# Kernel optimization log

Measured on AMD Instinct MI355X. Metric: run time of the kernel, lower is better.

## Reference

```python
import jax, jax.numpy as jnp
import numpy as np


NUM_HEADS = 16


def setup_inputs() -> dict:
    key = jax.random.key(0)
    ks = jax.random.split(key, 6)
    B, Sq, Skv, DQ, DKV = 2, 1024, 4096, 1024, 768
    return {
        "x_q": jax.random.normal(ks[0], (B, Sq, DQ), jnp.float32),
        "x_kv": jax.random.normal(ks[1], (B, Skv, DKV), jnp.float32),
        "Wq": jax.random.normal(ks[2], (DQ, DQ), jnp.float32) * 0.02,
        "Wk": jax.random.normal(ks[3], (DQ, DKV), jnp.float32) * 0.02,
        "Wv": jax.random.normal(ks[4], (DQ, DKV), jnp.float32) * 0.02,
        "Wo": jax.random.normal(ks[5], (DQ, DQ), jnp.float32) * 0.02,
    }


def _split_heads(x):
    # Faithful to torch view(B, H, S, hd): a pure reshape, NOT a transpose.
    B, S, D = x.shape
    return x.reshape(B, NUM_HEADS, S, D // NUM_HEADS)


def reference(x_q, x_kv, Wq, Wk, Wv, Wo):
    head_dim = x_q.shape[-1] // NUM_HEADS
    # torch Linear: y = x @ W.T, weight shape (out, in)
    Q = _split_heads(jnp.einsum("bsd,od->bso", x_q, Wq))   # (B,H,Sq',hd)
    K = _split_heads(jnp.einsum("bsd,od->bso", x_kv, Wk))  # (B,H,Skv',hd)
    V = _split_heads(jnp.einsum("bsd,od->bso", x_kv, Wv))
    # Scale is 1/head_dim (not 1/sqrt), faithful to the source.
    scores = jnp.einsum("bhqd,bhkd->bhqk", Q, K) / head_dim
    attn = jax.nn.softmax(scores, axis=-1)
    out = jnp.einsum("bhqk,bhkd->bhqd", attn, V)  # (B,H,Sq',hd)
    B, Sq, DQ = x_q.shape
    out = out.transpose(0, 2, 1, 3).reshape(B, Sq, DQ)
    return jnp.einsum("bsd,od->bso", out, Wo)
```

## Files before the change

### kernel.cpp

```cpp
#include <hip/hip_runtime.h>
#include <hip/hip_bf16.h>
#include <cstdint>

#define THREADS 256

typedef __attribute__((ext_vector_type(8))) short bf16x8;
typedef __attribute__((ext_vector_type(4))) float f32x4;
typedef __attribute__((ext_vector_type(2))) unsigned int u32x2;

__device__ __forceinline__ void load_lds16(const void* g, void* l) {
    __builtin_amdgcn_global_load_lds(
        (const __attribute__((address_space(1))) unsigned int*)g,
        (__attribute__((address_space(3))) unsigned int*)l, 16, 0, 0);
}

__device__ __forceinline__ unsigned short f2bf(float x) {
    __hip_bfloat16 hb = __float2bfloat16(x);
    return *(unsigned short*)&hb;
}

__device__ __forceinline__ unsigned cvt_pk_bf16(float lo, float hi) {
    unsigned r;
    asm("v_cvt_pk_bf16_f32 %0, %1, %2" : "=v"(r) : "v"(lo), "v"(hi));
    return r;
}

__device__ __forceinline__ float fexp2(float x) {
#if __has_builtin(__builtin_amdgcn_exp2f)
    return __builtin_amdgcn_exp2f(x);
#else
    return exp2f(x);
#endif
}

__device__ __forceinline__ void swap32(unsigned& lo, unsigned& hi) {
#if __has_builtin(__builtin_amdgcn_permlane32_swap)
    u32x2 r = __builtin_amdgcn_permlane32_swap(lo, hi, false, false);
    lo = r[0]; hi = r[1];
#else
    unsigned plo = (unsigned)__shfl_xor((int)lo, 32, 64);
    unsigned phi = (unsigned)__shfl_xor((int)hi, 32, 64);
    bool up = (threadIdx.x & 32) != 0;
    unsigned nlo = up ? phi : lo;
    unsigned nhi = up ? hi : plo;
    lo = nlo; hi = nhi;
#endif
}

__global__ __launch_bounds__(THREADS)
void cast_inputs(const float* __restrict__ xq, const float* __restrict__ xkv,
                 const float* __restrict__ wq, const float* __restrict__ wk,
                 const float* __restrict__ wv, const float* __restrict__ wo,
                 unsigned short* __restrict__ oq, unsigned short* __restrict__ okv,
                 unsigned short* __restrict__ owq, unsigned short* __restrict__ owk,
                 unsigned short* __restrict__ owv, unsigned short* __restrict__ owo) {
    const unsigned n0 = 524288, n1 = 1572864, n2 = 262144, n3 = 196608, n4 = 196608;
    unsigned i = blockIdx.x * THREADS + threadIdx.x;
    const float* src; unsigned short* dst; unsigned off;
    if (i < n0)                    { src = xq;  dst = oq;  off = i; }
    else if (i < n0+n1)            { src = xkv; dst = okv; off = i - n0; }
    else if (i < n0+n1+n2)         { src = wq;  dst = owq; off = i - n0 - n1; }
    else if (i < n0+n1+n2+n3)      { src = wk;  dst = owk; off = i - n0 - n1 - n2; }
    else if (i < n0+n1+n2+n3+n4)   { src = wv;  dst = owv; off = i - n0 - n1 - n2 - n3; }
    else                           { src = wo;  dst = owo; off = i - n0 - n1 - n2 - n3 - n4; }
    float4 v = *(const float4*)(src + (size_t)off * 4);
    ushort4 o;
    o.x = f2bf(v.x); o.y = f2bf(v.y); o.z = f2bf(v.z); o.w = f2bf(v.w);
    *(ushort4*)(dst + (size_t)off * 4) = o;
}

__global__ __launch_bounds__(THREADS)
void gemm_proj(const unsigned short* __restrict__ xkv, const unsigned short* __restrict__ wkv,
               unsigned short* __restrict__ Kn, unsigned short* __restrict__ Vt,
               const unsigned short* __restrict__ xq, const unsigned short* __restrict__ wq,
               unsigned short* __restrict__ Qout) {
    __shared__ __align__(16) unsigned short As[128 * 64];
    __shared__ __align__(16) unsigned short Bs[128 * 64];

    const int t    = threadIdx.x;
    const int w    = t >> 6;
    const int lane = t & 63;
    const int l15  = lane & 15;
    const int quad = lane >> 4;
    const int wm   = w & 1;
    const int wn   = w >> 1;

    if (blockIdx.x < 1024) {
        const int bN = (blockIdx.x & 15) * 128;
        const int bM = (blockIdx.x >> 4) * 128;
        const int Kd = 768;

        const int srow = t >> 3;
        const int scol = ((t & 7) ^ ((t >> 4) & 7)) << 3;
        const unsigned short* ga = xkv + (size_t)(bM + srow) * Kd + scol;
        const unsigned short* gb = wkv + (size_t)(bN + srow) * Kd + scol;
        const int lbase = w * 512;

        const int xr = (l15 >> 1) & 7;
        int aoff[2][4], boff[2][4];
#pragma unroll
        for (int kk = 0; kk < 2; ++kk)
#pragma unroll
            for (int mt = 0; mt < 4; ++mt) {
                aoff[kk][mt] = (wm * 64 + mt * 16 + l15) * 64 + (((kk * 4 + quad) ^ xr) << 3);
                boff[kk][mt] = (wn * 64 + mt * 16 + l15) * 64 + (((kk * 4 + quad) ^ xr) << 3);
            }

        f32x4 acc[4][4];
#pragma unroll
        for (int mt = 0; mt < 4; ++mt)
#pragma unroll
            for (int nt = 0; nt < 4; ++nt)
#pragma unroll
                for (int r = 0; r < 4; ++r) acc[mt][nt][r] = 0.f;

        for (int k0 = 0; k0 < Kd; k0 += 64) {
            __syncthreads();
#pragma unroll
            for (int it = 0; it < 4; ++it) {
                load_lds16(ga + (size_t)it * 32 * Kd + k0, &As[lbase + it * 2048]);
                load_lds16(gb + (size_t)it * 32 * Kd + k0, &Bs[lbase + it * 2048]);
            }
            __syncthreads();

#pragma unroll
            for (int kk = 0; kk < 2; ++kk) {
                bf16x8 af[4], bf[4];
#pragma unroll
                for (int mt = 0; mt < 4; ++mt) af[mt] = *(const bf16x8*)&As[aoff[kk][mt]];
#pragma unroll
                for (int nt = 0; nt < 4; ++nt) bf[nt] = *(const bf16x8*)&Bs[boff[kk][nt]];
#pragma unroll
                for (int mt = 0; mt < 4; ++mt)
#pragma unroll
                    for (int nt = 0; nt < 4; ++nt)
                        acc[mt][nt] = __builtin_amdgcn_mfma_f32_16x16x32_bf16(af[mt], bf[nt], acc[mt][nt], 0, 0, 0);
            }
        }

        const int rbase = bM + wm * 64;
        const int b  = rbase >> 12;
        const int h  = (rbase & 4095) >> 8;
        if (bN < 1024) {
            const int G = (bN + wn * 64) >> 6;
            unsigned short* kp = Kn + (size_t)(b * 16 + h) * 262144 + (size_t)G * 256 * 64 + l15;
#pragma unroll
            for (int mt = 0; mt < 4; ++mt)
#pragma unroll
                for (int r = 0; r < 4; ++r) {
                    int u = (rbase & 255) + mt * 16 + quad * 4 + r;
                    unsigned short* cp = kp + (size_t)u * 64;
#pragma unroll
                    for (int nt = 0; nt < 4; ++nt) cp[nt * 16] = f2bf(acc[mt][nt][r]);
                }
        } else {
            const int Gv = (bN - 1024 + wn * 64) >> 6;
            unsigned short* vp = Vt + (size_t)(b * 16 + h) * 262144 + (size_t)Gv * 256;
#pragma unroll
            for (int nt = 0; nt < 4; ++nt) {
                int d = nt * 16 + l15;
#pragma unroll
                for (int mt = 0; mt < 4; ++mt) {
                    int u = (rbase & 255) + mt * 16 + quad * 4;
                    ushort4 pk;
                    pk.x = f2bf(acc[mt][nt][0]);
                    pk.y = f2bf(acc[mt][nt][1]);
                    pk.z = f2bf(acc[mt][nt][2]);
                    pk.w = f2bf(acc[mt][nt][3]);
                    *(ushort4*)(vp + (size_t)d * 4096 + u) = pk;
                }
            }
        }
    } else {
        const int id = blockIdx.x - 1024;
        const int bN = (id & 15) * 64;
        const int bM = (id >> 4) * 64;
        const int Kd = 1024, N = 1024;

        const int srow = t >> 3;
        const int scol = ((t & 7) ^ ((t >> 3) & 7)) << 3;
        const unsigned short* ga = xq + (size_t)(bM + srow) * Kd + scol;
        const unsigned short* gb = wq + (size_t)(bN + srow) * Kd + scol;
        const int lbase = w * 512;

        int aoff[2][2], boff[2][2];
#pragma unroll
        for (int kk = 0; kk < 2; ++kk)
#pragma unroll
            for (int mt = 0; mt < 2; ++mt) {
                aoff[kk][mt] = (wm * 32 + mt * 16 + l15) * 64 + (((kk * 4 + quad) ^ (l15 & 7)) << 3);
                boff[kk][mt] = (wn * 32 + mt * 16 + l15) * 64 + (((kk * 4 + quad) ^ (l15 & 7)) << 3);
            }

        f32x4 acc[2][2];
#pragma unroll
        for (int mt = 0; mt < 2; ++mt)
#pragma unroll
            for (int nt = 0; nt < 2; ++nt)
#pragma unroll
                for (int r = 0; r < 4; ++r) acc[mt][nt][r] = 0.f;

        for (int k0 = 0; k0 < Kd; k0 += 64) {
            __syncthreads();
#pragma unroll
            for (int it = 0; it < 2; ++it) {
                load_lds16(ga + (size_t)it * 32 * Kd + k0, &As[lbase + it * 2048]);
                load_lds16(gb + (size_t)it * 32 * Kd + k0, &Bs[lbase + it * 2048]);
            }
            __syncthreads();

#pragma unroll
            for (int kk = 0; kk < 2; ++kk) {
                bf16x8 af[2], bf[2];
#pragma unroll
                for (int mt = 0; mt < 2; ++mt) af[mt] = *(const bf16x8*)&As[aoff[kk][mt]];
#pragma unroll
                for (int nt = 0; nt < 2; ++nt) bf[nt] = *(const bf16x8*)&Bs[boff[kk][nt]];
#pragma unroll
                for (int mt = 0; mt < 2; ++mt)
#pragma unroll
                    for (int nt = 0; nt < 2; ++nt)
                        acc[mt][nt] = __builtin_amdgcn_mfma_f32_16x16x32_bf16(af[mt], bf[nt], acc[mt][nt], 0, 0, 0);
            }
        }

#pragma unroll
        for (int mt = 0; mt < 2; ++mt)
#pragma unroll
            for (int r = 0; r < 4; ++r) {
                int row = bM + wm * 32 + mt * 16 + quad * 4 + r;
                int col = bN + wn * 32 + l15;
                unsigned short* cp = Qout + (size_t)row * N + col;
#pragma unroll
                for (int nt = 0; nt < 2; ++nt) cp[nt * 16] = f2bf(acc[mt][nt][r]);
            }
    }
}

template <bool OUTF32>
__global__ __launch_bounds__(THREADS)
void gemm_bf16_nt64(const unsigned short* __restrict__ A, const unsigned short* __restrict__ W,
                    void* __restrict__ Cout, int M, int N, int Kd) {
    __shared__ __align__(16) unsigned short As[64 * 64];
    __shared__ __align__(16) unsigned short Bs[64 * 64];

    const int t    = threadIdx.x;
    const int w    = t >> 6;
    const int lane = t & 63;
    const int l15  = lane & 15;
    const int quad = lane >> 4;
    const int wm   = w & 1;
    const int wn   = w >> 1;
    const int bM = blockIdx.y * 64;
    const int bN = blockIdx.x * 64;

    const int srow = t >> 3;
    const int scol = ((t & 7) ^ ((t >> 3) & 7)) << 3;
    const unsigned short* ga = A + (size_t)(bM + srow) * Kd + scol;
    const unsigned short* gb = W + (size_t)(bN + srow) * Kd + scol;
    const int lbase = w * 512;

    int aoff[2][2], boff[2][2];
#pragma unroll
    for (int kk = 0; kk < 2; ++kk)
#pragma unroll
        for (int mt = 0; mt < 2; ++mt) {
            aoff[kk][mt] = (wm * 32 + mt * 16 + l15) * 64 + (((kk * 4 + quad) ^ (l15 & 7)) << 3);
            boff[kk][mt] = (wn * 32 + mt * 16 + l15) * 64 + (((kk * 4 + quad) ^ (l15 & 7)) << 3);
        }

    f32x4 acc[2][2];
#pragma unroll
    for (int mt = 0; mt < 2; ++mt)
#pragma unroll
        for (int nt = 0; nt < 2; ++nt)
#pragma unroll
            for (int r = 0; r < 4; ++r) acc[mt][nt][r] = 0.f;

    for (int k0 = 0; k0 < Kd; k0 += 64) {
        __syncthreads();
#pragma unroll
        for (int it = 0; it < 2; ++it) {
            load_lds16(ga + (size_t)it * 32 * Kd + k0, &As[lbase + it * 2048]);
            load_lds16(gb + (size_t)it * 32 * Kd + k0, &Bs[lbase + it * 2048]);
        }
        __syncthreads();

#pragma unroll
        for (int kk = 0; kk < 2; ++kk) {
            bf16x8 af[2], bf[2];
#pragma unroll
            for (int mt = 0; mt < 2; ++mt) af[mt] = *(const bf16x8*)&As[aoff[kk][mt]];
#pragma unroll
            for (int nt = 0; nt < 2; ++nt) bf[nt] = *(const bf16x8*)&Bs[boff[kk][nt]];
#pragma unroll
            for (int mt = 0; mt < 2; ++mt)
#pragma unroll
                for (int nt = 0; nt < 2; ++nt)
                    acc[mt][nt] = __builtin_amdgcn_mfma_f32_16x16x32_bf16(af[mt], bf[nt], acc[mt][nt], 0, 0, 0);
        }
    }

#pragma unroll
    for (int mt = 0; mt < 2; ++mt)
#pragma unroll
        for (int r = 0; r < 4; ++r) {
            int row = bM + wm * 32 + mt * 16 + quad * 4 + r;
            int col = bN + wn * 32 + l15;
            if (OUTF32) {
                float* cp = (float*)Cout + (size_t)row * N + col;
#pragma unroll
                for (int nt = 0; nt < 2; ++nt) cp[nt * 16] = acc[mt][nt][r];
            } else {
                unsigned short* cp = (unsigned short*)Cout + (size_t)row * N + col;
#pragma unroll
                for (int nt = 0; nt < 2; ++nt) cp[nt * 16] = f2bf(acc[mt][nt][r]);
            }
        }
}

__global__ __launch_bounds__(THREADS, 2)
void attn_mfma10(const unsigned short* __restrict__ Q, const unsigned short* __restrict__ K,
                 const unsigned short* __restrict__ Vt, unsigned short* __restrict__ AO) {
    extern __shared__ __align__(16) unsigned short sm[];
    unsigned short* Ks = sm;
    unsigned short* Vs = sm + 8192;
    float* OS = (float*)sm;
    float* Lw = (float*)(sm + 26624);

    const int bid  = blockIdx.x;
    const int slot = bid >> 3;
    const int qq   = slot & 15;
    const int hh   = (bid & 7) + 8 * (slot >> 4);
    const int q0 = qq * 64;
    const int h  = hh & 15;
    const int b  = hh >> 4;

    const int t    = threadIdx.x;
    const int w    = t >> 6;
    const int lane = t & 63;
    const int l15  = lane & 15;
    const int quad = lane >> 4;
    const int qsel = quad & 1;

    const unsigned short* Qh = Q + (size_t)b * 1048576 + (size_t)h * 65536 + (size_t)q0 * 64;
    const unsigned short* Kh = K + (size_t)b * 4194304 + (size_t)h * 262144;
    const unsigned short* Vh = Vt + (size_t)(b * 16 + h) * 262144;

    bf16x8 Qb[4][2];
#pragma unroll
    for (int qt = 0; qt < 4; ++qt)
#pragma unroll
        for (int kk = 0; kk < 2; ++kk)
            Qb[qt][kk] = *(const bf16x8*)(Qh + (size_t)(qt * 16 + l15) * 64 + kk * 32 + quad * 8);

    const unsigned short* gKw = Kh + (size_t)(w * 32 + (lane >> 3)) * 64
                                   + (((lane & 7) ^ ((lane >> 3) & 7)) << 3);
    const unsigned short* gVw = Vh + (size_t)(lane >> 2) * 4096 + w * 32
                                   + (((lane & 3) ^ ((lane >> 2) & 3)) << 3);
    const int ldsK = w * 2048;
    const int ldsV = w * 2048;

    int koff[2][2];
#pragma unroll
    for (int kvt = 0; kvt < 2; ++kvt)
#pragma unroll
        for (int kk = 0; kk < 2; ++kk)
            koff[kvt][kk] = (w * 32 + kvt * 16 + l15) * 64 + (((kk * 4 + quad) ^ (l15 & 7)) << 3);
    int voff[4];
#pragma unroll
    for (int dt = 0; dt < 4; ++dt)
        voff[dt] = w * 2048 + (dt * 16 + l15) * 32 + ((quad ^ (l15 & 3)) << 3);

    f32x4 Oacc[4][4];
#pragma unroll
    for (int qt = 0; qt < 4; ++qt)
#pragma unroll
        for (int dt = 0; dt < 4; ++dt)
#pragma unroll
            for (int r = 0; r < 4; ++r) Oacc[qt][dt][r] = 0.f;
    float lsum[4] = {0.f, 0.f, 0.f, 0.f};

    const float e2s = 0.022542110013890053f;

#pragma unroll
    for (int it = 0; it < 4; ++it)
        load_lds16(gKw + it * 512, &Ks[ldsK + it * 512]);
#pragma unroll
    for (int it = 0; it < 4; ++it)
        load_lds16(gVw + (size_t)it * 65536, &Vs[ldsV + it * 512]);

    for (int kc = 0; kc < 32; ++kc) {
        const int kn = (kc + 1) & 31;

        asm volatile("s_waitcnt vmcnt(4)" ::: "memory");

        bf16x8 ka0 = *(const bf16x8*)&Ks[koff[0][0]];
        bf16x8 kb0 = *(const bf16x8*)&Ks[koff[0][1]];
        bf16x8 ka1 = *(const bf16x8*)&Ks[koff[1][0]];
        bf16x8 kb1 = *(const bf16x8*)&Ks[koff[1][1]];
        asm volatile("s_waitcnt lgkmcnt(0)" ::: "memory");
#pragma unroll
        for (int it = 0; it < 4; ++it)
            load_lds16(gKw + (size_t)kn * 8192 + it * 512, &Ks[ldsK + it * 512]);

        bf16x8 Pa[4];
#pragma unroll
        for (int qt = 0; qt < 4; ++qt) {
            f32x4 S0 = {0.f, 0.f, 0.f, 0.f};
            S0 = __builtin_amdgcn_mfma_f32_16x16x32_bf16(ka0, Qb[qt][0], S0, 0, 0, 0);
            S0 = __builtin_amdgcn_mfma_f32_16x16x32_bf16(kb0, Qb[qt][1], S0, 0, 0, 0);
            f32x4 S1 = {0.f, 0.f, 0.f, 0.f};
            S1 = __builtin_amdgcn_mfma_f32_16x16x32_bf16(ka1, Qb[qt][0], S1, 0, 0, 0);
            S1 = __builtin_amdgcn_mfma_f32_16x16x32_bf16(kb1, Qb[qt][1], S1, 0, 0, 0);
            float p0 = fexp2(S0[0] * e2s);
            float p1 = fexp2(S0[1] * e2s);
            float p2 = fexp2(S0[2] * e2s);
            float p3 = fexp2(S0[3] * e2s);
            float p4 = fexp2(S1[0] * e2s);
            float p5 = fexp2(S1[1] * e2s);
            float p6 = fexp2(S1[2] * e2s);
            float p7 = fexp2(S1[3] * e2s);
            lsum[qt] += ((p0 + p1) + (p2 + p3)) + ((p4 + p5) + (p6 + p7));
            unsigned ca = cvt_pk_bf16(p0, p1);
            unsigned cb = cvt_pk_bf16(p2, p3);
            unsigned cc = cvt_pk_bf16(p4, p5);
            unsigned cd = cvt_pk_bf16(p6, p7);
            swap32(ca, cc);
            swap32(cb, cd);
            unsigned r0 = (unsigned)__shfl_xor((int)(qsel ? ca : cc), 16, 64);
            unsigned r1 = (unsigned)__shfl_xor((int)(qsel ? cb : cd), 16, 64);
            union { unsigned u[4]; bf16x8 v; } pk_;
            pk_.u[0] = qsel ? r0 : ca;
            pk_.u[1] = qsel ? r1 : cb;
            pk_.u[2] = qsel ? cc : r0;
            pk_.u[3] = qsel ? cd : r1;
            Pa[qt] = pk_.v;
        }

        asm volatile("s_waitcnt vmcnt(4)" ::: "memory");

        bf16x8 Vf[4];
#pragma unroll
        for (int dt = 0; dt < 4; ++dt) Vf[dt] = *(const bf16x8*)&Vs[voff[dt]];
        asm volatile("s_waitcnt lgkmcnt(0)" ::: "memory");
#pragma unroll
        for (int it = 0; it < 4; ++it)
            load_lds16(gVw + (size_t)kn * 128 + (size_t)it * 65536, &Vs[ldsV + it * 512]);

        __builtin_amdgcn_s_setprio(1);
#pragma unroll
        for (int qt = 0; qt < 4; ++qt)
#pragma unroll
            for (int dt = 0; dt < 4; ++dt)
                Oacc[qt][dt] = __builtin_amdgcn_mfma_f32_16x16x32_bf16(Pa[qt], Vf[dt], Oacc[qt][dt], 0, 0, 0);
        __builtin_amdgcn_s_setprio(0);
    }

#pragma unroll
    for (int qt = 0; qt < 4; ++qt) {
        float v = lsum[qt];
        v += __shfl_xor(v, 16);
        v += __shfl_xor(v, 32);
        lsum[qt] = v;
    }
    __syncthreads();
    if (lane < 16) {
#pragma unroll
        for (int qt = 0; qt < 4; ++qt)
            Lw[w * 64 + qt * 16 + lane] = lsum[qt];
    }
    if (w > 0) {
        float* myOS = OS + (w - 1) * 4352;
#pragma unroll
        for (int qt = 0; qt < 4; ++qt)
#pragma unroll
            for (int dt = 0; dt < 4; ++dt)
                *(f32x4*)&myOS[(dt * 16 + l15) * 68 + qt * 16 + quad * 4] = Oacc[qt][dt];
    }
    __syncthreads();
    if (w == 0) {
#pragma unroll
        for (int qt = 0; qt < 4; ++qt) {
            f32x4 lv = *(const f32x4*)&Lw[qt * 16 + quad * 4];
            lv += *(const f32x4*)&Lw[64 + qt * 16 + quad * 4];
            lv += *(const f32x4*)&Lw[128 + qt * 16 + quad * 4];
            lv += *(const f32x4*)&Lw[192 + qt * 16 + quad * 4];
            f32x4 inv;
#pragma unroll
            for (int r = 0; r < 4; ++r) inv[r] = 1.0f / lv[r];
#pragma unroll
            for (int dt = 0; dt < 4; ++dt) {
                f32x4 o = Oacc[qt][dt];
                int os = (dt * 16 + l15) * 68 + qt * 16 + quad * 4;
                o += *(const f32x4*)&OS[os];
                o += *(const f32x4*)&OS[4352 + os];
                o += *(const f32x4*)&OS[8704 + os];
#pragma unroll
                for (int r = 0; r < 4; ++r) {
                    int q = qt * 16 + quad * 4 + r;
                    AO[(size_t)b * 1048576 + (size_t)(q0 + q) * 1024 + (h << 6) + dt * 16 + l15]
                        = f2bf(o[r] * inv[r]);
                }
            }
        }
    }
}

extern "C" void kernel_launch(void* const* d_in, const int* in_sizes, int n_in,
                              void* d_out, int out_size, void* d_ws, size_t ws_size,
                              hipStream_t stream) {
    const float* x_q  = (const float*)d_in[0];
    const float* x_kv = (const float*)d_in[1];
    const float* Wq   = (const float*)d_in[2];
    const float* Wk   = (const float*)d_in[3];
    const float* Wv   = (const float*)d_in[4];
    const float* Wo   = (const float*)d_in[5];
    float* out = (float*)d_out;

    unsigned short* base   = (unsigned short*)d_ws;
    unsigned short* xq_bf  = base;
    unsigned short* xkv_bf = base + 2097152;
    unsigned short* wq_bf  = base + 8388608;
    unsigned short* wk_bf  = base + 9437184;
    unsigned short* wv_bf  = base + 10223616;
    unsigned short* wo_bf  = base + 11010048;
    unsigned short* Qw     = base + 12058624;
    unsigned short* Kw     = base + 14155776;
    unsigned short* AOb    = base + 22544384;
    unsigned short* Vtw    = base + 30932992;

    dim3 blk(THREADS);
    cast_inputs<<<dim3(11776), blk, 0, stream>>>(x_q, x_kv, Wq, Wk, Wv, Wo,
                                                 xq_bf, xkv_bf, wq_bf, wk_bf, wv_bf, wo_bf);
    gemm_proj<<<dim3(1536), blk, 0, stream>>>(xkv_bf, wk_bf, Kw, Vtw, xq_bf, wq_bf, Qw);
    attn_mfma10<<<dim3(512), blk, 54272, stream>>>(Qw, Kw, Vtw, AOb);
    gemm_bf16_nt64<true><<<dim3(16, 32), blk, 0, stream>>>(AOb, wo_bf, (void*)out, 2048, 1024, 1024);
}
```

Measured before the change: 204.8 us.

## Split attention KV range in two with separate combine kernel

Attention now splits the KV sequence into two halves, launching 1024 blocks instead of 512. Each block writes unnormalized fp32 partial outputs and row sums to workspace, and a new combine kernel sums the halves, normalizes, and writes bf16. The change also reduces LDS use through a tree reduction across warps, raises launch bounds to 4 blocks per SM, and replaces the shuffle-based P repacking with permlane16 swaps. The aim is better occupancy and wave fill on the GPU, paid for with an extra launch and fp32 partial traffic that reuses the input-cast workspace region.

After: 278.3 us. +35.9%, slower.

```diff
diff --git a/kernel.cpp b/kernel.cpp
--- a/kernel.cpp
+++ b/kernel.cpp
@@ -44,6 +44,20 @@
     unsigned nlo = up ? phi : lo;
     unsigned nhi = up ? hi : plo;
     lo = nlo; hi = nhi;
+#endif
+}
+
+__device__ __forceinline__ void swap16(unsigned& a, unsigned& c) {
+#if __has_builtin(__builtin_amdgcn_permlane16_swap)
+    u32x2 r = __builtin_amdgcn_permlane16_swap(a, c, false, false);
+    a = r[0]; c = r[1];
+#else
+    unsigned as = (unsigned)__shfl_xor((int)a, 16, 64);
+    unsigned cs = (unsigned)__shfl_xor((int)c, 16, 64);
+    bool odd = (threadIdx.x & 16) != 0;
+    unsigned na = odd ? cs : a;
+    unsigned nc = odd ? c  : as;
+    a = na; c = nc;
 #endif
 }
 
@@ -319,33 +333,37 @@
         }
 }
 
-__global__ __launch_bounds__(THREADS, 2)
-void attn_mfma10(const unsigned short* __restrict__ Q, const unsigned short* __restrict__ K,
-                 const unsigned short* __restrict__ Vt, unsigned short* __restrict__ AO) {
+__global__ __launch_bounds__(THREADS, 4)
+void attn_mfma12(const unsigned short* __restrict__ Q, const unsigned short* __restrict__ K,
+                 const unsigned short* __restrict__ Vt,
+                 float* __restrict__ Opart, float* __restrict__ lpart) {
     extern __shared__ __align__(16) unsigned short sm[];
     unsigned short* Ks = sm;
     unsigned short* Vs = sm + 8192;
     float* OS = (float*)sm;
-    float* Lw = (float*)(sm + 26624);
+    float* Lw = OS + 8704;
 
     const int bid  = blockIdx.x;
-    const int slot = bid >> 3;
+    const int kvh  = bid >> 9;
+    const int bid9 = bid & 511;
+    const int slot = bid9 >> 3;
     const int qq   = slot & 15;
-    const int hh   = (bid & 7) + 8 * (slot >> 4);
+    const int hh   = (bid9 & 7) + 8 * (slot >> 4);
     const int q0 = qq * 64;
     const int h  = hh & 15;
     const int b  = hh >> 4;
+    const int pslot = kvh * 512 + bid9;
 
     const int t    = threadIdx.x;
     const int w    = t >> 6;
     const int lane = t & 63;
     const int l15  = lane & 15;
     const int quad = lane >> 4;
-    const int qsel = quad & 1;
 
     const unsigned short* Qh = Q + (size_t)b * 1048576 + (size_t)h * 65536 + (size_t)q0 * 64;
-    const unsigned short* Kh = K + (size_t)b * 4194304 + (size_t)h * 262144;
-    const unsigned short* Vh = Vt + (size_t)(b * 16 + h) * 262144;
+    const unsigned short* Kh = K + (size_t)b * 4194304 + (size_t)h * 262144
+                                 + (size_t)kvh * 131072;
+    const unsigned short* Vh = Vt + (size_t)(b * 16 + h) * 262144 + kvh * 2048;
 
     bf16x8 Qb[4][2];
 #pragma unroll
@@ -390,8 +408,8 @@
     for (int it = 0; it < 4; ++it)
         load_lds16(gVw + (size_t)it * 65536, &Vs[ldsV + it * 512]);
 
-    for (int kc = 0; kc < 32; ++kc) {
-        const int kn = (kc + 1) & 31;
+    for (int kc = 0; kc < 16; ++kc) {
+        const int kn = (kc + 1) & 15;
 
         asm volatile("s_waitcnt vmcnt(4)" ::: "memory");
 
@@ -428,13 +446,13 @@
             unsigned cd = cvt_pk_bf16(p6, p7);
             swap32(ca, cc);
             swap32(cb, cd);
-            unsigned r0 = (unsigned)__shfl_xor((int)(qsel ? ca : cc), 16, 64);
-            unsigned r1 = (unsigned)__shfl_xor((int)(qsel ? cb : cd), 16, 64);
+            swap16(ca, cc);
+            swap16(cb, cd);
             union { unsigned u[4]; bf16x8 v; } pk_;
-            pk_.u[0] = qsel ? r0 : ca;
-            pk_.u[1] = qsel ? r1 : cb;
-            pk_.u[2] = qsel ? cc : r0;
-            pk_.u[3] = qsel ? cd : r1;
+            pk_.u[0] = ca;
+            pk_.u[1] = cb;
+            pk_.u[2] = cc;
+            pk_.u[3] = cd;
             Pa[qt] = pk_.v;
         }
 
@@ -470,8 +488,8 @@
         for (int qt = 0; qt < 4; ++qt)
             Lw[w * 64 + qt * 16 + lane] = lsum[qt];
     }
-    if (w > 0) {
-        float* myOS = OS + (w - 1) * 4352;
+    if (w == 1 || w == 3) {
+        float* myOS = OS + (w >> 1) * 4352;
 #pragma unroll
         for (int qt = 0; qt < 4; ++qt)
 #pragma unroll
@@ -479,32 +497,70 @@
                 *(f32x4*)&myOS[(dt * 16 + l15) * 68 + qt * 16 + quad * 4] = Oacc[qt][dt];
     }
     __syncthreads();
+    if (w == 0 || w == 2) {
+        const float* srcOS = OS + (w >> 1) * 4352;
+#pragma unroll
+        for (int qt = 0; qt < 4; ++qt)
+#pragma unroll
+            for (int dt = 0; dt < 4; ++dt)
+                Oacc[qt][dt] += *(const f32x4*)&srcOS[(dt * 16 + l15) * 68 + qt * 16 + quad * 4];
+    }
+    __syncthreads();
+    if (w == 2) {
+#pragma unroll
+        for (int qt = 0; qt < 4; ++qt)
+#pragma unroll
+            for (int dt = 0; dt < 4; ++dt)
+                *(f32x4*)&OS[(dt * 16 + l15) * 68 + qt * 16 + quad * 4] = Oacc[qt][dt];
+    }
+    __syncthreads();
     if (w == 0) {
+        float* pO = Opart + (size_t)pslot * 4096;
+        float* pl = lpart + (size_t)pslot * 64;
 #pragma unroll
         for (int qt = 0; qt < 4; ++qt) {
             f32x4 lv = *(const f32x4*)&Lw[qt * 16 + quad * 4];
             lv += *(const f32x4*)&Lw[64 + qt * 16 + quad * 4];
             lv += *(const f32x4*)&Lw[128 + qt * 16 + quad * 4];
             lv += *(const f32x4*)&Lw[192 + qt * 16 + quad * 4];
-            f32x4 inv;
-#pragma unroll
-            for (int r = 0; r < 4; ++r) inv[r] = 1.0f / lv[r];
+            if (l15 == 0) *(f32x4*)&pl[qt * 16 + quad * 4] = lv;
 #pragma unroll
             for (int dt = 0; dt < 4; ++dt) {
                 f32x4 o = Oacc[qt][dt];
-                int os = (dt * 16 + l15) * 68 + qt * 16 + quad * 4;
-                o += *(const f32x4*)&OS[os];
-                o += *(const f32x4*)&OS[4352 + os];
-                o += *(const f32x4*)&OS[8704 + os];
-#pragma unroll
-                for (int r = 0; r < 4; ++r) {
-                    int q = qt * 16 + quad * 4 + r;
-                    AO[(size_t)b * 1048576 + (size_t)(q0 + q) * 1024 + (h << 6) + dt * 16 + l15]
-                        = f2bf(o[r] * inv[r]);
-                }
-            }
-        }
-    }
+                o += *(const f32x4*)&OS[(dt * 16 + l15) * 68 + qt * 16 + quad * 4];
+#pragma unroll
+                for (int r = 0; r < 4; ++r)
+                    pO[(size_t)(qt * 16 + quad * 4 + r) * 64 + dt * 16 + l15] = o[r];
+            }
+        }
+    }
+}
+
+__global__ __launch_bounds__(THREADS)
+void attn_combine(const float* __restrict__ Op, const float* __restrict__ lp,
+                  unsigned short* __restrict__ AO) {
+    const int t    = threadIdx.x;
+    const int s9   = blockIdx.x >> 2;
+    const int part = blockIdx.x & 3;
+    const int q    = part * 16 + (t >> 4);
+    const int dg   = (t & 15) << 2;
+    const int slot = s9 >> 3;
+    const int qq   = slot & 15;
+    const int hh   = (s9 & 7) + 8 * (slot >> 4);
+    const int q0 = qq * 64;
+    const int h  = hh & 15;
+    const int b  = hh >> 4;
+
+    size_t off = (size_t)s9 * 4096 + q * 64 + dg;
+    f32x4 a = *(const f32x4*)&Op[off];
+    f32x4 c = *(const f32x4*)&Op[2097152 + off];
+    float inv = 1.0f / (lp[s9 * 64 + q] + lp[32768 + s9 * 64 + q]);
+    ushort4 o;
+    o.x = f2bf((a[0] + c[0]) * inv);
+    o.y = f2bf((a[1] + c[1]) * inv);
+    o.z = f2bf((a[2] + c[2]) * inv);
+    o.w = f2bf((a[3] + c[3]) * inv);
+    *(ushort4*)(AO + (size_t)b * 1048576 + (size_t)(q0 + q) * 1024 + (h << 6) + dg) = o;
 }
 
 extern "C" void kernel_launch(void* const* d_in, const int* in_sizes, int n_in,
@@ -530,10 +586,14 @@
     unsigned short* AOb    = base + 22544384;
     unsigned short* Vtw    = base + 30932992;
 
+    float* Opart = (float*)d_ws;
+    float* lpart = (float*)(base + 24641536);
+
     dim3 blk(THREADS);
     cast_inputs<<<dim3(11776), blk, 0, stream>>>(x_q, x_kv, Wq, Wk, Wv, Wo,
                                                  xq_bf, xkv_bf, wq_bf, wk_bf, wv_bf, wo_bf);
     gemm_proj<<<dim3(1536), blk, 0, stream>>>(xkv_bf, wk_bf, Kw, Vtw, xq_bf, wq_bf, Qw);
-    attn_mfma10<<<dim3(512), blk, 54272, stream>>>(Qw, Kw, Vtw, AOb);
+    attn_mfma12<<<dim3(1024), blk, 35840, stream>>>(Qw, Kw, Vtw, Opart, lpart);
+    attn_combine<<<dim3(2048), blk, 0, stream>>>(Opart, lpart, AOb);
     gemm_bf16_nt64<true><<<dim3(16, 32), blk, 0, stream>>>(AOb, wo_bf, (void*)out, 2048, 1024, 1024);
 }
```

## Double-buffer K/V LDS tiles in attention and use permlane16 swap for P

Applied to the files above, without the earlier changes.

The attention kernel moves from single-buffered K and V LDS tiles to two buffers, prefetching chunk kc+2 while chunk kc is computed, and relaxes the vmcnt waits to match. It also replaces the shfl_xor-plus-select repacking of the probability fragments with a permlane16_swap. The aim is to hide global-to-LDS latency and cut cross-lane shuffle cost. LDS per block grows from 54 KB to 64 KB, which may limit occupancy to two blocks per CU, and the epilogue reuses the same shared memory.

Measured after the change: 194.8 us. 1.05x faster.

```diff
diff --git a/kernel.cpp b/kernel.cpp
--- a/kernel.cpp
+++ b/kernel.cpp
@@ -44,6 +44,20 @@
     unsigned nlo = up ? phi : lo;
     unsigned nhi = up ? hi : plo;
     lo = nlo; hi = nhi;
+#endif
+}
+
+__device__ __forceinline__ void swap16(unsigned& a, unsigned& c) {
+#if __has_builtin(__builtin_amdgcn_permlane16_swap)
+    u32x2 r = __builtin_amdgcn_permlane16_swap(a, c, false, false);
+    a = r[0]; c = r[1];
+#else
+    unsigned as = (unsigned)__shfl_xor((int)a, 16, 64);
+    unsigned cs = (unsigned)__shfl_xor((int)c, 16, 64);
+    bool odd = (threadIdx.x & 16) != 0;
+    unsigned na = odd ? cs : a;
+    unsigned nc = odd ? c  : as;
+    a = na; c = nc;
 #endif
 }
 
@@ -320,11 +334,9 @@
 }
 
 __global__ __launch_bounds__(THREADS, 2)
-void attn_mfma10(const unsigned short* __restrict__ Q, const unsigned short* __restrict__ K,
+void attn_mfma13(const unsigned short* __restrict__ Q, const unsigned short* __restrict__ K,
                  const unsigned short* __restrict__ Vt, unsigned short* __restrict__ AO) {
     extern __shared__ __align__(16) unsigned short sm[];
-    unsigned short* Ks = sm;
-    unsigned short* Vs = sm + 8192;
     float* OS = (float*)sm;
     float* Lw = (float*)(sm + 26624);
 
@@ -341,7 +353,6 @@
     const int lane = t & 63;
     const int l15  = lane & 15;
     const int quad = lane >> 4;
-    const int qsel = quad & 1;
 
     const unsigned short* Qh = Q + (size_t)b * 1048576 + (size_t)h * 65536 + (size_t)q0 * 64;
     const unsigned short* Kh = K + (size_t)b * 4194304 + (size_t)h * 262144;
@@ -385,24 +396,33 @@
 
 #pragma unroll
     for (int it = 0; it < 4; ++it)
-        load_lds16(gKw + it * 512, &Ks[ldsK + it * 512]);
+        load_lds16(gKw + it * 512, &sm[ldsK + it * 512]);
 #pragma unroll
     for (int it = 0; it < 4; ++it)
-        load_lds16(gVw + (size_t)it * 65536, &Vs[ldsV + it * 512]);
+        load_lds16(gVw + (size_t)it * 65536, &sm[16384 + ldsV + it * 512]);
+#pragma unroll
+    for (int it = 0; it < 4; ++it)
+        load_lds16(gKw + 8192 + it * 512, &sm[8192 + ldsK + it * 512]);
+#pragma unroll
+    for (int it = 0; it < 4; ++it)
+        load_lds16(gVw + 128 + (size_t)it * 65536, &sm[24576 + ldsV + it * 512]);
 
     for (int kc = 0; kc < 32; ++kc) {
-        const int kn = (kc + 1) & 31;
-
-        asm volatile("s_waitcnt vmcnt(4)" ::: "memory");
-
-        bf16x8 ka0 = *(const bf16x8*)&Ks[koff[0][0]];
-        bf16x8 kb0 = *(const bf16x8*)&Ks[koff[0][1]];
-        bf16x8 ka1 = *(const bf16x8*)&Ks[koff[1][0]];
-        bf16x8 kb1 = *(const bf16x8*)&Ks[koff[1][1]];
+        const int buf = kc & 1;
+        const int kn2 = (kc + 2) & 31;
+        const int kbase = buf * 8192;
+        const int vbase = 16384 + buf * 8192;
+
+        asm volatile("s_waitcnt vmcnt(12)" ::: "memory");
+
+        bf16x8 ka0 = *(const bf16x8*)&sm[kbase + koff[0][0]];
+        bf16x8 kb0 = *(const bf16x8*)&sm[kbase + koff[0][1]];
+        bf16x8 ka1 = *(const bf16x8*)&sm[kbase + koff[1][0]];
+        bf16x8 kb1 = *(const bf16x8*)&sm[kbase + koff[1][1]];
         asm volatile("s_waitcnt lgkmcnt(0)" ::: "memory");
 #pragma unroll
         for (int it = 0; it < 4; ++it)
-            load_lds16(gKw + (size_t)kn * 8192 + it * 512, &Ks[ldsK + it * 512]);
+            load_lds16(gKw + (size_t)kn2 * 8192 + it * 512, &sm[kbase + ldsK + it * 512]);
 
         bf16x8 Pa[4];
 #pragma unroll
@@ -428,25 +448,25 @@
             unsigned cd = cvt_pk_bf16(p6, p7);
             swap32(ca, cc);
             swap32(cb, cd);
-            unsigned r0 = (unsigned)__shfl_xor((int)(qsel ? ca : cc), 16, 64);
-            unsigned r1 = (unsigned)__shfl_xor((int)(qsel ? cb : cd), 16, 64);
+            swap16(ca, cc);
+            swap16(cb, cd);
             union { unsigned u[4]; bf16x8 v; } pk_;
-            pk_.u[0] = qsel ? r0 : ca;
-            pk_.u[1] = qsel ? r1 : cb;
-            pk_.u[2] = qsel ? cc : r0;
-            pk_.u[3] = qsel ? cd : r1;
+            pk_.u[0] = ca;
+            pk_.u[1] = cb;
+            pk_.u[2] = cc;
+            pk_.u[3] = cd;
             Pa[qt] = pk_.v;
         }
 
-        asm volatile("s_waitcnt vmcnt(4)" ::: "memory");
+        asm volatile("s_waitcnt vmcnt(12)" ::: "memory");
 
         bf16x8 Vf[4];
 #pragma unroll
-        for (int dt = 0; dt < 4; ++dt) Vf[dt] = *(const bf16x8*)&Vs[voff[dt]];
+        for (int dt = 0; dt < 4; ++dt) Vf[dt] = *(const bf16x8*)&sm[vbase + voff[dt]];
         asm volatile("s_waitcnt lgkmcnt(0)" ::: "memory");
 #pragma unroll
         for (int it = 0; it < 4; ++it)
-            load_lds16(gVw + (size_t)kn * 128 + (size_t)it * 65536, &Vs[ldsV + it * 512]);
+            load_lds16(gVw + (size_t)kn2 * 128 + (size_t)it * 65536, &sm[vbase + ldsV + it * 512]);
 
         __builtin_amdgcn_s_setprio(1);
 #pragma unroll
@@ -534,6 +554,6 @@
     cast_inputs<<<dim3(11776), blk, 0, stream>>>(x_q, x_kv, Wq, Wk, Wv, Wo,
                                                  xq_bf, xkv_bf, wq_bf, wk_bf, wv_bf, wo_bf);
     gemm_proj<<<dim3(1536), blk, 0, stream>>>(xkv_bf, wk_bf, Kw, Vtw, xq_bf, wq_bf, Qw);
-    attn_mfma10<<<dim3(512), blk, 54272, stream>>>(Qw, Kw, Vtw, AOb);
+    attn_mfma13<<<dim3(512), blk, 65536, stream>>>(Qw, Kw, Vtw, AOb);
     gemm_bf16_nt64<true><<<dim3(16, 32), blk, 0, stream>>>(AOb, wo_bf, (void*)out, 2048, 1024, 1024);
 }
```
